# Optimization experiments

Measured on AMD Instinct MI355X. Metric: run time of the kernel, lower is better.

The kernel has to match this reference:

```python
import jax, jax.numpy as jnp
import numpy as np

N_UNARY = 16
N_BINARY = 4
N_NODES = 100000
N_EDGES = 1600000
N_CLAUSES = 8

# Parsed unary clauses: clause i = nU{i}, U{i+1}, U{i+2}
U_IDX = np.array([[i, i + 1, i + 2] for i in range(N_CLAUSES)], dtype=np.int32)
U_SGN = np.tile(np.array([[-1.0, 1.0, 1.0]], dtype=np.float32), (N_CLAUSES, 1))
# Parsed binary clauses over joined matrix [Ux(0:16), Uy(16:32), B(32:36)]:
# clause i = nU{i}x, B{i%4}, U{i}y
B_IDX = np.array([[i, 32 + (i % 4), 16 + i] for i in range(N_CLAUSES)], dtype=np.int32)
B_SGN = np.tile(np.array([[-1.0, 1.0, 1.0]], dtype=np.float32), (N_CLAUSES, 1))


def knowledge_enhancer(x, idx, sgn, w):
    """KENN clause deltas: gather literal columns, softmax(signs*x), scatter-add.
    x: [n, width], idx/sgn: [n_clauses, 3], w: [n_clauses] -> delta [n, width]."""
    sel = x[:, idx] * sgn  # [n, n_clauses, 3]
    d = (w[:, None] * sgn) * jax.nn.softmax(sel, axis=-1)  # [n, n_clauses, 3]
    return jnp.zeros_like(x).at[:, idx].add(d)


def setup_inputs() -> dict:
    key = jax.random.key(0)
    k1, k2, k3, k4 = jax.random.split(key, 4)
    unary = jax.random.normal(k1, (N_NODES, N_UNARY), dtype=jnp.float32)
    binary = jax.random.normal(k2, (N_EDGES, N_BINARY), dtype=jnp.float32)
    index1 = jax.random.randint(k3, (N_EDGES,), 0, N_NODES)
    index2 = jax.random.randint(k4, (N_EDGES,), 0, N_NODES)
    unary_cw = jnp.full((N_CLAUSES,), 0.5, dtype=jnp.float32)
    binary_cw = jnp.full((N_CLAUSES,), 0.5, dtype=jnp.float32)
    return {"unary": unary, "binary": binary, "unary_cw": unary_cw,
            "binary_cw": binary_cw, "index1": index1, "index2": index2}


def reference(unary, binary, unary_cw, binary_cw, index1, index2):
    # Unary knowledge enhancement
    u = unary + knowledge_enhancer(unary, U_IDX, U_SGN, unary_cw)
    # Join: gather endpoint unary features, concat with binary preactivations
    joined = jnp.concatenate([u[index1], u[index2], binary], axis=1)  # [E, 36]
    db = knowledge_enhancer(joined, B_IDX, B_SGN, binary_cw)  # [E, 36]
    # GroupBy: scatter unary parts back to nodes, keep binary part on edges
    delta_up = (jnp.zeros_like(u)
                .at[index1].add(db[:, :N_UNARY])
                .at[index2].add(db[:, N_UNARY:2 * N_UNARY]))
    delta_bp = db[:, 2 * N_UNARY:]
    # activation is identity (default lambda x: x)
    return u + delta_up, binary + delta_bp
```

## Files before the change

kernel.cpp:

```cpp
#include <hip/hip_runtime.h>
#include <math.h>


#define NU 16
#define NC 8
#define TILE_N 400u
#define NB 512
#define BT 512
#define CACHE_N 3200
#define ACC_ST 400

__device__ __forceinline__ int q10(float x) {
    int q = __float2int_rn(x * 512.0f);
    q = q < -511 ? -511 : (q > 511 ? 511 : q);
    return q & 0x3FF;
}
__device__ __forceinline__ int sx10(unsigned w, int sh) {
    return ((int)(w << (22 - sh))) >> 22;
}
__device__ __forceinline__ unsigned long long pk4(int a0, int a1, int a2, int a3) {
    return (unsigned long long)(long long)a0 +
           ((unsigned long long)(long long)a1 << 16) +
           ((unsigned long long)(long long)a2 << 32) +
           ((unsigned long long)(unsigned short)a3 << 48);
}

__global__ void unary_enhance_kernel(const float* __restrict__ unary,
                                     const float* __restrict__ ucw,
                                     float* __restrict__ out_u,
                                     float* __restrict__ u_lo,
                                     int n_nodes) {
    int n = blockIdx.x * blockDim.x + threadIdx.x;
    if (n >= n_nodes) return;

    float x[NU];
    const float4* src = (const float4*)(unary + (size_t)n * NU);
#pragma unroll
    for (int j = 0; j < 4; ++j) {
        float4 v = src[j];
        x[4*j+0] = v.x; x[4*j+1] = v.y; x[4*j+2] = v.z; x[4*j+3] = v.w;
    }
    float dlt[NU];
#pragma unroll
    for (int j = 0; j < NU; ++j) dlt[j] = 0.0f;
#pragma unroll
    for (int i = 0; i < NC; ++i) {
        float w = ucw[i];
        float a = -x[i], b = x[i+1], c = x[i+2];
        float m = fmaxf(a, fmaxf(b, c));
        float e0 = __expf(a - m);
        float e1 = __expf(b - m);
        float e2 = __expf(c - m);
        float inv = 1.0f / (e0 + e1 + e2);
        dlt[i]   -= w * e0 * inv;
        dlt[i+1] += w * e1 * inv;
        dlt[i+2] += w * e2 * inv;
    }
    float u[NU];
#pragma unroll
    for (int j = 0; j < NU; ++j) u[j] = x[j] + dlt[j];

    float4* dst = (float4*)(out_u + (size_t)n * NU);
#pragma unroll
    for (int j = 0; j < 4; ++j) {
        float4 v; v.x = u[4*j+0]; v.y = u[4*j+1]; v.z = u[4*j+2]; v.w = u[4*j+3];
        dst[j] = v;
    }
    float4* lo = (float4*)(u_lo + (size_t)n * 8);
    float4 l0; l0.x = u[0]; l0.y = u[1]; l0.z = u[2]; l0.w = u[3];
    float4 l1; l1.x = u[4]; l1.y = u[5]; l1.z = u[6]; l1.w = u[7];
    lo[0] = l0; lo[1] = l1;
}

__global__ __launch_bounds__(BT, 8)
void bin_edges_kernel(const float* __restrict__ binary,
                      const float* __restrict__ bcw,
                      const int* __restrict__ index1,
                      const int* __restrict__ index2,
                      const float* __restrict__ u_lo,
                      float* __restrict__ out_b,
                      unsigned* __restrict__ cursor,
                      uint4* __restrict__ entries,
                      float* __restrict__ out_u,
                      int n_edges, int T, int cap, int chunk) {
    __shared__ unsigned hist[256];
    __shared__ int ic1[CACHE_N];
    __shared__ int ic2[CACHE_N];
    int tid = threadIdx.x;
    for (int t = tid; t < T; t += BT) hist[t] = 0u;
    __syncthreads();

    int e0 = blockIdx.x * chunk;
    int e1 = e0 + chunk; if (e1 > n_edges) e1 = n_edges;

    for (int e = e0 + tid; e < e1; e += BT) {
        int i1 = index1[e];
        int i2 = index2[e];
        int l = e - e0;
        ic1[l] = i1;
        ic2[l] = i2;
        atomicAdd(&hist[(unsigned)i1 / TILE_N], 1u);
        atomicAdd(&hist[(unsigned)i2 / TILE_N], 1u);
    }
    __syncthreads();

    for (int t = tid; t < T; t += BT) {
        unsigned c = hist[t];
        unsigned base = 0u;
        if (c) base = atomicAdd(&cursor[t], c);
        hist[t] = base;
    }
    __syncthreads();

    float w[NC];
#pragma unroll
    for (int i = 0; i < NC; ++i) w[i] = bcw[i];

    for (int e = e0 + tid; e < e1; e += BT) {
        int l = e - e0;
        int i1 = ic1[l];
        int i2 = ic2[l];
        float4 bv = ((const float4*)binary)[e];
        float b[4] = {bv.x, bv.y, bv.z, bv.w};

        const float4* p1 = (const float4*)(u_lo + (size_t)i1 * 8);
        float4 a0 = p1[0], a1 = p1[1];
        const float4* p2 = (const float4*)(u_lo + (size_t)i2 * 8);
        float4 c0 = p2[0], c1 = p2[1];
        float u1[8] = {a0.x,a0.y,a0.z,a0.w,a1.x,a1.y,a1.z,a1.w};
        float u2[8] = {c0.x,c0.y,c0.z,c0.w,c1.x,c1.y,c1.z,c1.w};

        float d1[8], d2[8], dbp[4] = {0.f,0.f,0.f,0.f};
#pragma unroll
        for (int i = 0; i < NC; ++i) {
            float a = -u1[i], bb = b[i & 3], c = u2[i];
            float m = fmaxf(a, fmaxf(bb, c));
            float e0x = __expf(a - m);
            float e1x = __expf(bb - m);
            float e2x = __expf(c - m);
            float inv = 1.0f / (e0x + e1x + e2x);
            d1[i] = -w[i] * e0x * inv;
            d2[i] =  w[i] * e2x * inv;
            dbp[i & 3] += w[i] * e1x * inv;
        }
        float4 ob;
        ob.x = b[0] + dbp[0];
        ob.y = b[1] + dbp[1];
        ob.z = b[2] + dbp[2];
        ob.w = b[3] + dbp[3];
        ((float4*)out_b)[e] = ob;

        unsigned t1 = (unsigned)i1 / TILE_N;
        unsigned id1 = (unsigned)i1 - t1 * TILE_N;
        unsigned slot1 = atomicAdd(&hist[t1], 1u);
        if (slot1 < (unsigned)cap) {
            uint4 v;
            v.x = (unsigned)q10(d1[0]) | ((unsigned)q10(d1[1]) << 10) | ((unsigned)q10(d1[2]) << 20);
            v.y = (unsigned)q10(d1[3]) | ((unsigned)q10(d1[4]) << 10) | ((unsigned)q10(d1[5]) << 20);
            v.z = (unsigned)q10(d1[6]) | ((unsigned)q10(d1[7]) << 10) | (id1 << 20);
            v.w = 0u;
            entries[(size_t)t1 * cap + slot1] = v;
        } else {
            float* r = out_u + (size_t)i1 * NU;
#pragma unroll
            for (int i = 0; i < NC; ++i) atomicAdd(r + i, d1[i]);
        }

        unsigned t2 = (unsigned)i2 / TILE_N;
        unsigned id2 = (unsigned)i2 - t2 * TILE_N;
        unsigned slot2 = atomicAdd(&hist[t2], 1u);
        if (slot2 < (unsigned)cap) {
            uint4 v;
            v.x = (unsigned)q10(d2[0]) | ((unsigned)q10(d2[1]) << 10) | ((unsigned)q10(d2[2]) << 20);
            v.y = (unsigned)q10(d2[3]) | ((unsigned)q10(d2[4]) << 10) | ((unsigned)q10(d2[5]) << 20);
            v.z = (unsigned)q10(d2[6]) | ((unsigned)q10(d2[7]) << 10) | (id2 << 20);
            v.w = 0u;
            entries[(size_t)t2 * cap + slot2] = v;
        } else {
            float* r = out_u + (size_t)i2 * NU;
#pragma unroll
            for (int i = 0; i < NC; ++i) atomicAdd(r + i, d2[i]);
        }
    }
}

__global__ __launch_bounds__(512, 4)
void tile_acc_kernel(const unsigned* __restrict__ cursor,
                     const uint4* __restrict__ entries,
                     float* __restrict__ out_u,
                     int n_nodes, int cap) {
    __shared__ unsigned long long acc[2 * ACC_ST];
    int t = blockIdx.x;
    int tid = threadIdx.x;
    for (int i = tid; i < 2 * ACC_ST; i += 512) acc[i] = 0ull;
    __syncthreads();

    unsigned cnt = cursor[t];
    if (cnt > (unsigned)cap) cnt = (unsigned)cap;
    size_t base = (size_t)t * cap;

    unsigned cnt4 = cnt & ~3u;
    for (unsigned i = (unsigned)tid * 4; i < cnt4; i += 512 * 4) {
        uint4 v0 = entries[base + i + 0];
        uint4 v1 = entries[base + i + 1];
        uint4 v2 = entries[base + i + 2];
        uint4 v3 = entries[base + i + 3];
        uint4 vv[4] = {v0, v1, v2, v3};
#pragma unroll
        for (int k = 0; k < 4; ++k) {
            uint4 v = vv[k];
            unsigned id = v.z >> 20;
            unsigned long long lo = pk4(sx10(v.x, 0), sx10(v.x, 10), sx10(v.x, 20), sx10(v.y, 0));
            unsigned long long hi = pk4(sx10(v.y, 10), sx10(v.y, 20), sx10(v.z, 0), sx10(v.z, 10));
            atomicAdd(&acc[id], lo);
            atomicAdd(&acc[ACC_ST + id], hi);
        }
    }
    for (unsigned i = cnt4 + tid; i < cnt; i += 512) {
        uint4 v = entries[base + i];
        unsigned id = v.z >> 20;
        unsigned long long lo = pk4(sx10(v.x, 0), sx10(v.x, 10), sx10(v.x, 20), sx10(v.y, 0));
        unsigned long long hi = pk4(sx10(v.y, 10), sx10(v.y, 20), sx10(v.z, 0), sx10(v.z, 10));
        atomicAdd(&acc[id], lo);
        atomicAdd(&acc[ACC_ST + id], hi);
    }
    __syncthreads();

    const float INV = 1.0f / 512.0f;
    int nbase = t * (int)TILE_N;
    for (int l = tid; l < (int)TILE_N; l += 512) {
        int n = nbase + l;
        if (n >= n_nodes) continue;
        float col[8];
#pragma unroll
        for (int wd = 0; wd < 2; ++wd) {
            unsigned long long S = acc[wd*ACC_ST + l];
#pragma unroll
            for (int f = 0; f < 4; ++f) {
                short s = (short)(S & 0xFFFFull);
                col[wd*4 + f] = (float)s * INV;
                S = (S - (unsigned long long)(long long)s) >> 16;
            }
        }
        float4* row = (float4*)(out_u + (size_t)n * NU);
        float4 r0 = row[0], r1 = row[1];
        r0.x += col[0]; r0.y += col[1]; r0.z += col[2]; r0.w += col[3];
        r1.x += col[4]; r1.y += col[5]; r1.z += col[6]; r1.w += col[7];
        row[0] = r0; row[1] = r1;
    }
}

__global__ void edge_enhance_kernel(const float* __restrict__ binary,
                                    const float* __restrict__ bcw,
                                    const int* __restrict__ index1,
                                    const int* __restrict__ index2,
                                    const float* __restrict__ u_lo,
                                    float* __restrict__ out_u,
                                    float* __restrict__ out_b,
                                    int n_edges) {
    int e = blockIdx.x * blockDim.x + threadIdx.x;
    if (e >= n_edges) return;

    int i1 = index1[e];
    int i2 = index2[e];
    float4 bv = ((const float4*)binary)[e];
    float b[4] = {bv.x, bv.y, bv.z, bv.w};

    const float4* p1 = (const float4*)(u_lo + (size_t)i1 * 8);
    float4 a0 = p1[0], a1 = p1[1];
    const float4* p2 = (const float4*)(u_lo + (size_t)i2 * 8);
    float4 c0 = p2[0], c1 = p2[1];
    float u1[8] = {a0.x,a0.y,a0.z,a0.w,a1.x,a1.y,a1.z,a1.w};
    float u2[8] = {c0.x,c0.y,c0.z,c0.w,c1.x,c1.y,c1.z,c1.w};

    float d1[8], d2[8], dbp[4] = {0.f,0.f,0.f,0.f};
#pragma unroll
    for (int i = 0; i < NC; ++i) {
        float w = bcw[i];
        float a = -u1[i], bb = b[i & 3], c = u2[i];
        float m = fmaxf(a, fmaxf(bb, c));
        float e0 = __expf(a - m);
        float e1 = __expf(bb - m);
        float e2 = __expf(c - m);
        float inv = 1.0f / (e0 + e1 + e2);
        d1[i] = -w * e0 * inv;
        d2[i] =  w * e2 * inv;
        dbp[i & 3] += w * e1 * inv;
    }
    float* r1 = out_u + (size_t)i1 * NU;
#pragma unroll
    for (int i = 0; i < NC; ++i) atomicAdd(r1 + i, d1[i]);
    float* r2 = out_u + (size_t)i2 * NU;
#pragma unroll
    for (int i = 0; i < NC; ++i) atomicAdd(r2 + i, d2[i]);

    float4 ob;
    ob.x = b[0] + dbp[0];
    ob.y = b[1] + dbp[1];
    ob.z = b[2] + dbp[2];
    ob.w = b[3] + dbp[3];
    ((float4*)out_b)[e] = ob;
}

extern "C" void kernel_launch(void* const* d_in, const int* in_sizes, int n_in,
                              void* d_out, int out_size, void* d_ws, size_t ws_size,
                              hipStream_t stream) {
    const float* unary  = (const float*)d_in[0];
    const float* binary = (const float*)d_in[1];
    const float* ucw    = (const float*)d_in[2];
    const float* bcw    = (const float*)d_in[3];
    const int*   index1 = (const int*)d_in[4];
    const int*   index2 = (const int*)d_in[5];

    int n_nodes = in_sizes[0] / NU;
    int n_edges = in_sizes[4];

    float* out_u = (float*)d_out;
    float* out_b = out_u + (size_t)n_nodes * NU;

    int T = (int)(((unsigned)n_nodes + TILE_N - 1) / TILE_N);
    size_t mean = (2ull * (size_t)n_edges) / (size_t)T;
    int cap = (int)(mean + mean / 8 + 512);
    cap = (cap + 3) & ~3;

    int chunk = (n_edges + NB - 1) / NB;

    size_t u_lo_bytes  = (size_t)n_nodes * 8 * sizeof(float);
    size_t ent_off     = (u_lo_bytes + 15) & ~(size_t)15;
    size_t ent_bytes   = (size_t)T * cap * sizeof(uint4);
    size_t cur_off     = ent_off + ent_bytes;
    size_t cur_bytes   = (size_t)T * 4;
    size_t need        = cur_off + cur_bytes;

    float* u_lo = (float*)d_ws;
    uint4* entries = (uint4*)((char*)d_ws + ent_off);
    unsigned* cursor = (unsigned*)((char*)d_ws + cur_off);

    int tb = 256;
    unary_enhance_kernel<<<(n_nodes + tb - 1) / tb, tb, 0, stream>>>(
        unary, ucw, out_u, u_lo, n_nodes);

    if (ws_size >= need && T <= 256 && chunk <= CACHE_N) {
        (void)hipMemsetAsync(cursor, 0, cur_bytes, stream);
        bin_edges_kernel<<<NB, BT, 0, stream>>>(
            binary, bcw, index1, index2, u_lo, out_b,
            cursor, entries, out_u, n_edges, T, cap, chunk);
        tile_acc_kernel<<<T, 512, 0, stream>>>(
            cursor, entries, out_u, n_nodes, cap);
    } else {
        edge_enhance_kernel<<<(n_edges + tb - 1) / tb, tb, 0, stream>>>(
            binary, bcw, index1, index2, u_lo, out_u, out_b, n_edges);
    }
}
```

Baseline: 201.6 us.

## Fuse unary, binning, and tile accumulation into one cooperative kernel with grid syncs

Replaces the unary kernel, memset, binning kernel and tile-accumulate kernel with a single cooperative launch. Phases are separated by grid.sync(), which removes launch gaps and the memset. It also halves the node tile size so there are 500 tiles spread over the 512 blocks, and it tightens the per-tile capacity slack. The costs are grid-wide barriers, lower occupancy from the larger shared footprint (launch bounds drop to 4), and more tiles, which may overflow into the global-atomic fallback path.

```diff
diff --git a/kernel.cpp b/kernel.cpp
--- a/kernel.cpp
+++ b/kernel.cpp
@@ -1,14 +1,18 @@
 #include <hip/hip_runtime.h>
+#include <hip/hip_cooperative_groups.h>
 #include <math.h>
+
+namespace cg = cooperative_groups;
 
 
 #define NU 16
 #define NC 8
-#define TILE_N 400u
+#define TILE_N 200u
 #define NB 512
 #define BT 512
 #define CACHE_N 3200
-#define ACC_ST 400
+#define ACC_ST 200
+#define MAXT 512
 
 __device__ __forceinline__ int q10(float x) {
     int q = __float2int_rn(x * 512.0f);
@@ -25,14 +29,10 @@
            ((unsigned long long)(unsigned short)a3 << 48);
 }
 
-__global__ void unary_enhance_kernel(const float* __restrict__ unary,
-                                     const float* __restrict__ ucw,
-                                     float* __restrict__ out_u,
-                                     float* __restrict__ u_lo,
-                                     int n_nodes) {
-    int n = blockIdx.x * blockDim.x + threadIdx.x;
-    if (n >= n_nodes) return;
-
+__device__ __forceinline__ void unary_row(const float* __restrict__ unary,
+                                          const float* __restrict__ ucw,
+                                          float* __restrict__ out_u,
+                                          float* __restrict__ u_lo, int n) {
     float x[NU];
     const float4* src = (const float4*)(unary + (size_t)n * NU);
 #pragma unroll
@@ -72,22 +72,35 @@
     lo[0] = l0; lo[1] = l1;
 }
 
-__global__ __launch_bounds__(BT, 8)
-void bin_edges_kernel(const float* __restrict__ binary,
-                      const float* __restrict__ bcw,
-                      const int* __restrict__ index1,
-                      const int* __restrict__ index2,
-                      const float* __restrict__ u_lo,
-                      float* __restrict__ out_b,
-                      unsigned* __restrict__ cursor,
-                      uint4* __restrict__ entries,
-                      float* __restrict__ out_u,
-                      int n_edges, int T, int cap, int chunk) {
-    __shared__ unsigned hist[256];
+__global__ __launch_bounds__(BT, 4)
+void fused_kernel(const float* __restrict__ unary,
+                  const float* __restrict__ binary,
+                  const float* __restrict__ ucw,
+                  const float* __restrict__ bcw,
+                  const int* __restrict__ index1,
+                  const int* __restrict__ index2,
+                  float* __restrict__ out_u,
+                  float* __restrict__ out_b,
+                  float* __restrict__ u_lo,
+                  unsigned* __restrict__ cursor,
+                  uint4* __restrict__ entries,
+                  int n_nodes, int n_edges, int T, int cap, int chunk) {
+    __shared__ unsigned hist[MAXT];
     __shared__ int ic1[CACHE_N];
     __shared__ int ic2[CACHE_N];
+    __shared__ unsigned long long accbuf[2 * ACC_ST];
+
+    cg::grid_group grid = cg::this_grid();
     int tid = threadIdx.x;
-    for (int t = tid; t < T; t += BT) hist[t] = 0u;
+
+    for (int n = blockIdx.x * BT + tid; n < n_nodes; n += NB * BT) {
+        unary_row(unary, ucw, out_u, u_lo, n);
+    }
+    for (int t = blockIdx.x * BT + tid; t < T; t += NB * BT) cursor[t] = 0u;
+
+    grid.sync();
+
+    for (int t = tid; t < MAXT; t += BT) hist[t] = 0u;
     __syncthreads();
 
     int e0 = blockIdx.x * chunk;
@@ -182,72 +195,79 @@
             for (int i = 0; i < NC; ++i) atomicAdd(r + i, d2[i]);
         }
     }
-}
-
-__global__ __launch_bounds__(512, 4)
-void tile_acc_kernel(const unsigned* __restrict__ cursor,
-                     const uint4* __restrict__ entries,
-                     float* __restrict__ out_u,
-                     int n_nodes, int cap) {
-    __shared__ unsigned long long acc[2 * ACC_ST];
-    int t = blockIdx.x;
-    int tid = threadIdx.x;
-    for (int i = tid; i < 2 * ACC_ST; i += 512) acc[i] = 0ull;
-    __syncthreads();
-
-    unsigned cnt = cursor[t];
-    if (cnt > (unsigned)cap) cnt = (unsigned)cap;
-    size_t base = (size_t)t * cap;
-
-    unsigned cnt4 = cnt & ~3u;
-    for (unsigned i = (unsigned)tid * 4; i < cnt4; i += 512 * 4) {
-        uint4 v0 = entries[base + i + 0];
-        uint4 v1 = entries[base + i + 1];
-        uint4 v2 = entries[base + i + 2];
-        uint4 v3 = entries[base + i + 3];
-        uint4 vv[4] = {v0, v1, v2, v3};
-#pragma unroll
-        for (int k = 0; k < 4; ++k) {
-            uint4 v = vv[k];
+
+    grid.sync();
+
+    if (blockIdx.x < T) {
+        int t = blockIdx.x;
+        for (int i = tid; i < 2 * ACC_ST; i += BT) accbuf[i] = 0ull;
+        __syncthreads();
+
+        unsigned cnt = cursor[t];
+        if (cnt > (unsigned)cap) cnt = (unsigned)cap;
+        size_t base = (size_t)t * cap;
+
+        unsigned cnt4 = cnt & ~3u;
+        for (unsigned i = (unsigned)tid * 4; i < cnt4; i += BT * 4) {
+            uint4 v0 = entries[base + i + 0];
+            uint4 v1 = entries[base + i + 1];
+            uint4 v2 = entries[base + i + 2];
+            uint4 v3 = entries[base + i + 3];
+            uint4 vv[4] = {v0, v1, v2, v3};
+#pragma unroll
+            for (int k = 0; k < 4; ++k) {
+                uint4 v = vv[k];
+                unsigned id = v.z >> 20;
+                unsigned long long lo = pk4(sx10(v.x, 0), sx10(v.x, 10), sx10(v.x, 20), sx10(v.y, 0));
+                unsigned long long hi = pk4(sx10(v.y, 10), sx10(v.y, 20), sx10(v.z, 0), sx10(v.z, 10));
+                atomicAdd(&accbuf[id], lo);
+                atomicAdd(&accbuf[ACC_ST + id], hi);
+            }
+        }
+        for (unsigned i = cnt4 + tid; i < cnt; i += BT) {
+            uint4 v = entries[base + i];
             unsigned id = v.z >> 20;
             unsigned long long lo = pk4(sx10(v.x, 0), sx10(v.x, 10), sx10(v.x, 20), sx10(v.y, 0));
             unsigned long long hi = pk4(sx10(v.y, 10), sx10(v.y, 20), sx10(v.z, 0), sx10(v.z, 10));
-            atomicAdd(&acc[id], lo);
-            atomicAdd(&acc[ACC_ST + id], hi);
-        }
-    }
-    for (unsigned i = cnt4 + tid; i < cnt; i += 512) {
-        uint4 v = entries[base + i];
-        unsigned id = v.z >> 20;
-        unsigned long long lo = pk4(sx10(v.x, 0), sx10(v.x, 10), sx10(v.x, 20), sx10(v.y, 0));
-        unsigned long long hi = pk4(sx10(v.y, 10), sx10(v.y, 20), sx10(v.z, 0), sx10(v.z, 10));
-        atomicAdd(&acc[id], lo);
-        atomicAdd(&acc[ACC_ST + id], hi);
-    }
-    __syncthreads();
-
-    const float INV = 1.0f / 512.0f;
-    int nbase = t * (int)TILE_N;
-    for (int l = tid; l < (int)TILE_N; l += 512) {
-        int n = nbase + l;
-        if (n >= n_nodes) continue;
-        float col[8];
-#pragma unroll
-        for (int wd = 0; wd < 2; ++wd) {
-            unsigned long long S = acc[wd*ACC_ST + l];
-#pragma unroll
-            for (int f = 0; f < 4; ++f) {
-                short s = (short)(S & 0xFFFFull);
-                col[wd*4 + f] = (float)s * INV;
-                S = (S - (unsigned long long)(long long)s) >> 16;
+            atomicAdd(&accbuf[id], lo);
+            atomicAdd(&accbuf[ACC_ST + id], hi);
+        }
+        __syncthreads();
+
+        const float INV = 1.0f / 512.0f;
+        int nbase = t * (int)TILE_N;
+        for (int l = tid; l < (int)TILE_N; l += BT) {
+            int n = nbase + l;
+            if (n >= n_nodes) continue;
+            float col[8];
+#pragma unroll
+            for (int wd = 0; wd < 2; ++wd) {
+                unsigned long long S = accbuf[wd*ACC_ST + l];
+#pragma unroll
+                for (int f = 0; f < 4; ++f) {
+                    short s = (short)(S & 0xFFFFull);
+                    col[wd*4 + f] = (float)s * INV;
+                    S = (S - (unsigned long long)(long long)s) >> 16;
+                }
             }
-        }
-        float4* row = (float4*)(out_u + (size_t)n * NU);
-        float4 r0 = row[0], r1 = row[1];
-        r0.x += col[0]; r0.y += col[1]; r0.z += col[2]; r0.w += col[3];
-        r1.x += col[4]; r1.y += col[5]; r1.z += col[6]; r1.w += col[7];
-        row[0] = r0; row[1] = r1;
-    }
+            float4* row = (float4*)(out_u + (size_t)n * NU);
+            float4 r0 = row[0], r1 = row[1];
+            r0.x += col[0]; r0.y += col[1]; r0.z += col[2]; r0.w += col[3];
+            r1.x += col[4]; r1.y += col[5]; r1.z += col[6]; r1.w += col[7];
+            row[0] = r0; row[1] = r1;
+        }
+    }
+}
+
+
+__global__ void unary_enhance_kernel(const float* __restrict__ unary,
+                                     const float* __restrict__ ucw,
+                                     float* __restrict__ out_u,
+                                     float* __restrict__ u_lo,
+                                     int n_nodes) {
+    int n = blockIdx.x * blockDim.x + threadIdx.x;
+    if (n >= n_nodes) return;
+    unary_row(unary, ucw, out_u, u_lo, n);
 }
 
 __global__ void edge_enhance_kernel(const float* __restrict__ binary,
@@ -320,7 +340,7 @@
 
     int T = (int)(((unsigned)n_nodes + TILE_N - 1) / TILE_N);
     size_t mean = (2ull * (size_t)n_edges) / (size_t)T;
-    int cap = (int)(mean + mean / 8 + 512);
+    int cap = (int)(mean + mean / 16 + 256);
     cap = (cap + 3) & ~3;
 
     int chunk = (n_edges + NB - 1) / NB;
@@ -336,19 +356,23 @@
     uint4* entries = (uint4*)((char*)d_ws + ent_off);
     unsigned* cursor = (unsigned*)((char*)d_ws + cur_off);
 
+    bool fast = (ws_size >= need && T <= MAXT && chunk <= CACHE_N);
+
+    if (fast) {
+        void* args[] = {
+            (void*)&unary, (void*)&binary, (void*)&ucw, (void*)&bcw,
+            (void*)&index1, (void*)&index2, (void*)&out_u, (void*)&out_b,
+            (void*)&u_lo, (void*)&cursor, (void*)&entries,
+            (void*)&n_nodes, (void*)&n_edges, (void*)&T, (void*)&cap, (void*)&chunk
+        };
+        hipError_t err = hipLaunchCooperativeKernel(
+            (const void*)fused_kernel, dim3(NB), dim3(BT), args, 0u, stream);
+        if (err == hipSuccess) return;
+    }
+
     int tb = 256;
     unary_enhance_kernel<<<(n_nodes + tb - 1) / tb, tb, 0, stream>>>(
         unary, ucw, out_u, u_lo, n_nodes);
-
-    if (ws_size >= need && T <= 256 && chunk <= CACHE_N) {
-        (void)hipMemsetAsync(cursor, 0, cur_bytes, stream);
-        bin_edges_kernel<<<NB, BT, 0, stream>>>(
-            binary, bcw, index1, index2, u_lo, out_b,
-            cursor, entries, out_u, n_edges, T, cap, chunk);
-        tile_acc_kernel<<<T, 512, 0, stream>>>(
-            cursor, entries, out_u, n_nodes, cap);
-    } else {
-        edge_enhance_kernel<<<(n_edges + tb - 1) / tb, tb, 0, stream>>>(
-            binary, bcw, index1, index2, u_lo, out_u, out_b, n_edges);
-    }
-}
+    edge_enhance_kernel<<<(n_edges + tb - 1) / tb, tb, 0, stream>>>(
+        binary, bcw, index1, index2, u_lo, out_u, out_b, n_edges);
+}
```

After: 342.6 us. 1.7x slower.
